# Performance work log

Measured on AMD Instinct MI355X. Metric: run time of the kernel, lower is better.

## Reference

```python
import jax, jax.numpy as jnp
import numpy as np


def setup_inputs() -> dict:
    key = jax.random.key(0)
    ks = jax.random.split(key, 8)
    bs, nq, jd = 16, 100, 51  # 3 * 17 joints
    return {
        "pred_conf": jax.random.normal(ks[0], (bs, nq, 1), jnp.float32),
        "pred_joint": jax.random.normal(ks[1], (bs, nq, jd), jnp.float32),
        "pred_action": jax.random.normal(ks[2], (bs, nq, 8), jnp.float32),
        "pred_identity": jax.random.normal(ks[3], (bs, nq, 10), jnp.float32),
        "tar_conf": jax.random.uniform(ks[4], (bs, nq), jnp.float32),
        "tar_joint": jax.random.normal(ks[5], (bs, nq, jd), jnp.float32),
        "tar_action": jax.random.randint(ks[6], (bs, nq), 0, 8, dtype=jnp.int32),
        "tar_identity": jax.random.randint(ks[7], (bs, nq), 0, 10, dtype=jnp.int32),
    }


def reference(pred_conf, pred_joint, pred_action, pred_identity,
              tar_conf, tar_joint, tar_action, tar_identity):
    # cost weights (defaults in __init__)
    cost_class = cost_joint = cost_action = cost_identity = 1.0
    bs, nq = pred_conf.shape[:2]
    N = bs * nq

    # --- C_prob: outer binary cross-entropy between sigmoid(pred_conf)[i] and tar_conf[j]
    p = jax.nn.sigmoid(pred_conf).reshape(N)          # [N]
    t = tar_conf.reshape(N)                            # [N]
    log_p = jnp.log(p)
    log_1mp = jnp.log1p(-p)
    C_prob = -(t[None, :] * log_p[:, None] + (1.0 - t[None, :]) * log_1mp[:, None])  # [N,N]

    # --- C_joint: L1 cdist between predicted and target joints
    oj = pred_joint.reshape(N, -1)                     # [N,51]
    tj = tar_joint.reshape(N, -1)                      # [N,51]
    C_joint = jnp.sum(jnp.abs(oj[:, None, :] - tj[None, :, :]), axis=-1)  # [N,N]

    # --- C_action / C_identity: computeCE with pred.shape[1] > 1 always targets class 0,
    # so the cost is column-constant: -log_softmax(pred[i])[0] broadcast over j.
    ce_a = -jax.nn.log_softmax(pred_action.reshape(N, -1), axis=-1)[:, 0]    # [N]
    ce_i = -jax.nn.log_softmax(pred_identity.reshape(N, -1), axis=-1)[:, 0]  # [N]

    C = (cost_class * C_prob
         + cost_joint * C_joint
         + (cost_action * ce_a + cost_identity * ce_i)[:, None])  # [N,N]

    # C.view(bs, nq, -1).split(nq, -1) then c[i] selects the (b, b) diagonal block
    Cb = C.reshape(bs, nq, bs, nq)
    blocks = Cb[jnp.arange(bs), :, jnp.arange(bs), :]  # [bs, nq, nq]
    return blocks
```

## Files before the change

### kernel.cpp

```cpp
#include <hip/hip_runtime.h>
#include <math.h>

constexpr int BS = 16;
constexpr int NQ = 100;
constexpr int JD = 51;
constexpr int NA = 8;
constexpr int NI = 10;
constexpr int ITILE = 10;
constexpr int NTILES = NQ / ITILE;
constexpr int BLOCK = 256;

__global__ __launch_bounds__(BLOCK) void matcher_kernel(
    const float* __restrict__ pred_conf,
    const float* __restrict__ pred_joint,
    const float* __restrict__ pred_action,
    const float* __restrict__ pred_ident,
    const float* __restrict__ tar_conf,
    const float* __restrict__ tar_joint,
    float* __restrict__ out)
{
    const int b   = blockIdx.x;
    const int it  = blockIdx.y;
    const int i0  = it * ITILE;
    const int tid = threadIdx.x;

    __shared__ float tjs[NQ * JD];
    __shared__ float pjs[ITILE][JD];
    __shared__ float lps[ITILE];
    __shared__ float l1ps[ITILE];
    __shared__ float rowc[ITILE];

    const float* tj_g = tar_joint + (size_t)b * NQ * JD;
    for (int idx = tid; idx < NQ * JD; idx += BLOCK) tjs[idx] = tj_g[idx];

    const float* pj_g = pred_joint + ((size_t)b * NQ + i0) * JD;
    for (int idx = tid; idx < ITILE * JD; idx += BLOCK) ((float*)pjs)[idx] = pj_g[idx];

    if (tid < ITILE) {
        const int row = b * NQ + i0 + tid;
        float x  = pred_conf[row];
        float lp = -log1pf(__expf(-x));
        lps[tid]  = lp;
        l1ps[tid] = lp - x;

        const float* a = pred_action + (size_t)row * NA;
        float m = a[0];
        #pragma unroll
        for (int k = 1; k < NA; k++) m = fmaxf(m, a[k]);
        float s = 0.f;
        #pragma unroll
        for (int k = 0; k < NA; k++) s += __expf(a[k] - m);
        float cea = __logf(s) + m - a[0];

        const float* pi = pred_ident + (size_t)row * NI;
        float m2 = pi[0];
        #pragma unroll
        for (int k = 1; k < NI; k++) m2 = fmaxf(m2, pi[k]);
        float s2 = 0.f;
        #pragma unroll
        for (int k = 0; k < NI; k++) s2 += __expf(pi[k] - m2);
        float cei = __logf(s2) + m2 - pi[0];

        rowc[tid] = cea + cei;
    }
    __syncthreads();

    const int j  = tid & 127;
    const int ih = tid >> 7;
    if (j < NQ) {
        float tj[JD];
        #pragma unroll
        for (int k = 0; k < JD; k++) tj[k] = tjs[j * JD + k];

        const float t = tar_conf[b * NQ + j];

        float* outp = out + ((size_t)b * NQ + i0) * NQ + j;
        const int il_beg = ih * (ITILE / 2);
        #pragma unroll
        for (int il = il_beg; il < il_beg + ITILE / 2; il++) {
            float s = 0.f;
            #pragma unroll
            for (int k = 0; k < JD; k++) s += fabsf(pjs[il][k] - tj[k]);
            float cp = -(t * lps[il] + (1.f - t) * l1ps[il]);
            outp[(size_t)il * NQ] = cp + s + rowc[il];
        }
    }
}

extern "C" void kernel_launch(void* const* d_in, const int* in_sizes, int n_in,
                              void* d_out, int out_size, void* d_ws, size_t ws_size,
                              hipStream_t stream) {
    const float* pred_conf   = (const float*)d_in[0];
    const float* pred_joint  = (const float*)d_in[1];
    const float* pred_action = (const float*)d_in[2];
    const float* pred_ident  = (const float*)d_in[3];
    const float* tar_conf    = (const float*)d_in[4];
    const float* tar_joint   = (const float*)d_in[5];
    float* outp = (float*)d_out;

    dim3 grid(BS, NTILES);
    matcher_kernel<<<grid, BLOCK, 0, stream>>>(
        pred_conf, pred_joint, pred_action, pred_ident, tar_conf, tar_joint, outp);
}
```

Before: 74.65 us.

## Shrink row tile, vectorize shared-memory staging, split L1 accumulation chains

Reduces the row tile from 10 to 4, raising the grid from 160 to 400 blocks so more of the GPU's compute units have work. Global-to-shared copies of target and predicted joints now use float4 loads; the offsets stay 16-byte aligned for these shapes. The per-pair L1 sum uses four independent accumulators to shorten the serial add chain. In exchange, each block re-stages the full 20 KB target joint tile for fewer output rows, so total L2 traffic goes up, and the changed summation order shifts floating-point rounding slightly.

After: 71.66 us. 1.04x faster.

```diff
diff --git a/kernel.cpp b/kernel.cpp
--- a/kernel.cpp
+++ b/kernel.cpp
@@ -6,7 +6,7 @@
 constexpr int JD = 51;
 constexpr int NA = 8;
 constexpr int NI = 10;
-constexpr int ITILE = 10;
+constexpr int ITILE = 4;
 constexpr int NTILES = NQ / ITILE;
 constexpr int BLOCK = 256;
 
@@ -24,17 +24,24 @@
     const int i0  = it * ITILE;
     const int tid = threadIdx.x;
 
-    __shared__ float tjs[NQ * JD];
-    __shared__ float pjs[ITILE][JD];
+    __shared__ __align__(16) float tjs[NQ * JD];
+    __shared__ __align__(16) float pjs[ITILE * JD];
     __shared__ float lps[ITILE];
     __shared__ float l1ps[ITILE];
     __shared__ float rowc[ITILE];
 
-    const float* tj_g = tar_joint + (size_t)b * NQ * JD;
-    for (int idx = tid; idx < NQ * JD; idx += BLOCK) tjs[idx] = tj_g[idx];
+    {
+        const float4* tj4 = (const float4*)(tar_joint + (size_t)b * NQ * JD);
+        float4* tjs4 = (float4*)tjs;
+        #pragma unroll
+        for (int idx = tid; idx < (NQ * JD) / 4; idx += BLOCK)
+            tjs4[idx] = tj4[idx];
 
-    const float* pj_g = pred_joint + ((size_t)b * NQ + i0) * JD;
-    for (int idx = tid; idx < ITILE * JD; idx += BLOCK) ((float*)pjs)[idx] = pj_g[idx];
+        const float4* pj4 = (const float4*)(pred_joint + ((size_t)b * NQ + i0) * JD);
+        float4* pjs4 = (float4*)pjs;
+        if (tid < (ITILE * JD) / 4)
+            pjs4[tid] = pj4[tid];
+    }
 
     if (tid < ITILE) {
         const int row = b * NQ + i0 + tid;
@@ -78,9 +85,18 @@
         const int il_beg = ih * (ITILE / 2);
         #pragma unroll
         for (int il = il_beg; il < il_beg + ITILE / 2; il++) {
-            float s = 0.f;
+            float s0 = 0.f, s1 = 0.f, s2 = 0.f, s3 = 0.f;
             #pragma unroll
-            for (int k = 0; k < JD; k++) s += fabsf(pjs[il][k] - tj[k]);
+            for (int k = 0; k + 3 < JD; k += 4) {
+                s0 += fabsf(pjs[il * JD + k + 0] - tj[k + 0]);
+                s1 += fabsf(pjs[il * JD + k + 1] - tj[k + 1]);
+                s2 += fabsf(pjs[il * JD + k + 2] - tj[k + 2]);
+                s3 += fabsf(pjs[il * JD + k + 3] - tj[k + 3]);
+            }
+            s0 += fabsf(pjs[il * JD + 48] - tj[48]);
+            s1 += fabsf(pjs[il * JD + 49] - tj[49]);
+            s2 += fabsf(pjs[il * JD + 50] - tj[50]);
+            float s = (s0 + s1) + (s2 + s3);
             float cp = -(t * lps[il] + (1.f - t) * l1ps[il]);
             outp[(size_t)il * NQ] = cp + s + rowc[il];
         }
```
